# Performance work log

Hardware: AMD Instinct MI355X
Metric: run time of the kernel (lower is better)

## Reference

```python
import jax, jax.numpy as jnp
import numpy as np

FORGET_BIAS = 1.0  # TF BasicLSTMCell default


def setup_inputs() -> dict:
    key = jax.random.key(0)
    k1, k2, k3 = jax.random.split(key, 3)
    B, T, F, H = 4096, 512, 32, 60
    x = jax.random.normal(k1, (B, T, F), dtype=jnp.float32)
    # BasicLSTMCell kernel: [F+H, 4H], gate order i, j, f, o
    kernel = jax.random.normal(k2, (F + H, 4 * H), dtype=jnp.float32) * 0.1
    bias = jnp.zeros((4 * H,), dtype=jnp.float32)
    dense_w = jax.random.normal(k3, (H, 1), dtype=jnp.float32) * 0.1
    dense_b = jnp.zeros((1,), dtype=jnp.float32)
    return {"x": x, "kernel": kernel, "bias": bias,
            "dense_w": dense_w, "dense_b": dense_b}


def reference(x, kernel, bias, dense_w, dense_b):
    B, T, F = x.shape
    H = dense_w.shape[0]

    def step(carry, x_t):
        c, h = carry  # each [B, H]
        gates = jnp.concatenate([x_t, h], axis=1) @ kernel + bias  # [B, 4H]
        i, j, f, o = jnp.split(gates, 4, axis=1)
        new_c = c * jax.nn.sigmoid(f + FORGET_BIAS) + jax.nn.sigmoid(i) * jnp.tanh(j)
        new_h = jnp.tanh(new_c) * jax.nn.sigmoid(o)
        return (new_c, new_h), None

    c0 = jnp.zeros((B, H), dtype=x.dtype)
    h0 = jnp.zeros((B, H), dtype=x.dtype)
    xs = jnp.transpose(x, (1, 0, 2))  # [T, B, F]
    (c, h), _ = jax.lax.scan(step, (c0, h0), xs)
    return h @ dense_w + dense_b  # [B, 1]
```

## Files before the change

### kernel.cpp

```cpp
#include <hip/hip_runtime.h>

typedef short short8  __attribute__((ext_vector_type(8)));
typedef float f32x4   __attribute__((ext_vector_type(4)));

#define B_TOTAL 4096
#define T_STEPS 512
#define F_IN    32
#define H_DIM   60
#define KW      92
#define BC      16
#define HPITCH  72

#define MFMA(A, B, C) __builtin_amdgcn_mfma_f32_16x16x32_bf16((A), (B), (C), 0, 0, 0)

__device__ __forceinline__ unsigned short bf16rne(float f) {
    unsigned int u = __float_as_uint(f);
    u += 0x7FFFu + ((u >> 16) & 1u);
    return (unsigned short)(u >> 16);
}
__device__ __forceinline__ float bf16tof(unsigned short s) {
    return __uint_as_float(((unsigned int)s) << 16);
}
__device__ __forceinline__ float rcpf(float z) {
    return __builtin_amdgcn_rcpf(z);
}
__device__ __forceinline__ float exp2f_(float z) {
#if __has_builtin(__builtin_amdgcn_exp2f)
    return __builtin_amdgcn_exp2f(z);
#else
    float r; asm("v_exp_f32 %0, %1" : "=v"(r) : "v"(z)); return r;
#endif
}

#define BAR()                                                                   \
    {                                                                           \
        asm volatile("s_waitcnt lgkmcnt(0)" ::: "memory");                      \
        __builtin_amdgcn_sched_barrier(0);                                      \
        __builtin_amdgcn_s_barrier();                                           \
        __builtin_amdgcn_sched_barrier(0);                                      \
    }

#define CVTH(VA, VB, OH)                                                        \
    {                                                                           \
        int4 hp;                                                                \
        asm("v_cvt_pk_bf16_f32 %0, %1, %2" : "=v"(hp.x) : "v"((VA).x), "v"((VA).y)); \
        asm("v_cvt_pk_bf16_f32 %0, %1, %2" : "=v"(hp.y) : "v"((VA).z), "v"((VA).w)); \
        asm("v_cvt_pk_bf16_f32 %0, %1, %2" : "=v"(hp.z) : "v"((VB).x), "v"((VB).y)); \
        asm("v_cvt_pk_bf16_f32 %0, %1, %2" : "=v"(hp.w) : "v"((VB).z), "v"((VB).w)); \
        OH = __builtin_bit_cast(short8, hp);                                    \
    }

#define CELL2(P, Q, H0, H1)                                                     \
    float h0, h1;                                                               \
    {                                                                           \
        float ei0 = exp2f_(-P[0]), ei1 = exp2f_(-Q[0]);                         \
        float qj0 = exp2f_(P[1]),  qj1 = exp2f_(Q[1]);                          \
        float ef0 = exp2f_(-P[2]), ef1 = exp2f_(-Q[2]);                         \
        float D10 = (1.0f + ei0) * (qj0 + 1.0f);                                \
        float D11 = (1.0f + ei1) * (qj1 + 1.0f);                                \
        float r1  = rcpf(D10 * D11);                                            \
        float D20 = 1.0f + ef0, D21 = 1.0f + ef1;                               \
        float r2  = rcpf(D20 * D21);                                            \
        cst0 = cst0 * (D21 * r2) + (qj0 - 1.0f) * (D11 * r1);                   \
        cst1 = cst1 * (D20 * r2) + (qj1 - 1.0f) * (D10 * r1);                   \
        float zc0 = __builtin_amdgcn_fmed3f(cst0 * (2.0f * 1.44269504088896340736f), -126.0f, 126.0f); \
        float zc1 = __builtin_amdgcn_fmed3f(cst1 * (2.0f * 1.44269504088896340736f), -126.0f, 126.0f); \
        float qc0 = exp2f_(zc0), qc1 = exp2f_(zc1);                             \
        float eo0 = exp2f_(-P[3]), eo1 = exp2f_(-Q[3]);                         \
        H0 = (qc0 - 1.0f) * rcpf((qc0 + 1.0f) * (1.0f + eo0));                  \
        H1 = (qc1 - 1.0f) * rcpf((qc1 + 1.0f) * (1.0f + eo1));                  \
    }

__global__ __launch_bounds__(512, 2)
void lstm_mfma_kernel(const float* __restrict__ x,
                      const float* __restrict__ wk,
                      const float* __restrict__ bias,
                      const float* __restrict__ dense_w,
                      const float* __restrict__ dense_b,
                      float* __restrict__ out)
{
    __shared__ __align__(16) short Hhi[2][BC][HPITCH];
    __shared__ float Hf[BC][64];

    const int tid  = threadIdx.x;
    const int lane = tid & 63;
    const int w    = tid >> 6;
    const int b0   = blockIdx.x * BC;
    const int lm   = lane & 15;
    const int kg   = lane >> 4;
    const int lk8  = kg * 8;

    const float LOG2E = 1.44269504088896340736f;

    short8 wh[2][3], wl[2][3];
    f32x4  biasv[2];
    #pragma unroll
    for (int tt = 0; tt < 2; ++tt) {
        const int mt = 2 * w + tt;
        if (mt < 15) {
            const int uo = 4 * mt + kg;
            f32x4 bv;
            #pragma unroll
            for (int r = 0; r < 4; ++r) {
                const float sc = (r == 1) ? 2.0f * LOG2E : LOG2E;
                bv[r] = (bias[r * 60 + uo] + (r == 2 ? 1.0f : 0.0f)) * sc;
            }
            biasv[tt] = bv;
            const int c = 16 * mt + lm;
            const int u = c >> 2, g = c & 3;
            const float gsc = (g == 1) ? 2.0f * LOG2E : LOG2E;
            #pragma unroll
            for (int s = 0; s < 3; ++s) {
                short8 hv, lv;
                #pragma unroll
                for (int e = 0; e < 8; ++e) {
                    const int k = s * 32 + lk8 + e;
                    float wv = (k < KW) ? wk[k * 240 + g * 60 + u] * gsc : 0.0f;
                    unsigned short hh = bf16rne(wv);
                    hv[e] = (short)hh;
                    lv[e] = (short)bf16rne(wv - bf16tof(hh));
                }
                wh[tt][s] = hv;
                wl[tt][s] = lv;
            }
        } else {
            biasv[tt] = (f32x4){0.f, 0.f, 0.f, 0.f};
            #pragma unroll
            for (int s = 0; s < 3; ++s) { wh[tt][s] = (short8)0; wl[tt][s] = (short8)0; }
        }
    }
    const int u0 = 8 * w + kg;
    const int u1 = 8 * w + 4 + kg;
    const bool t1ok = (2 * w + 1 < 15);

    for (int i = tid; i < 2 * BC * HPITCH; i += 512)
        (&Hhi[0][0][0])[i] = 0;

    const float* xrow = x + (size_t)(b0 + lm) * (T_STEPS * F_IN) + lk8;
    float4 va0 = *reinterpret_cast<const float4*>(xrow);
    float4 vb0 = *reinterpret_cast<const float4*>(xrow + 4);
    short8 axh;
    CVTH(va0, vb0, axh)
    float4 sBa = *reinterpret_cast<const float4*>(xrow + 1 * F_IN);
    float4 sBb = *reinterpret_cast<const float4*>(xrow + 1 * F_IN + 4);
    float4 sAa, sAb;
    const float* xp2 = xrow + 2 * F_IN;

    float cst0 = 0.f, cst1 = 0.f;
    __syncthreads();

#define STEPX(CUR, NXT, DOLOAD, LA, LB, XOFF, DOCVT, CA, CB, LASTF)             \
    {                                                                           \
        short8 uh1 = *reinterpret_cast<const short8*>(&Hhi[CUR][lm][lk8]);      \
        short8 uh2 = *reinterpret_cast<const short8*>(&Hhi[CUR][lm][32 + lk8]); \
        if (DOLOAD) {                                                           \
            LA = *reinterpret_cast<const float4*>(xp2 + (XOFF));                \
            LB = *reinterpret_cast<const float4*>(xp2 + (XOFF) + 4);            \
        }                                                                       \
        __builtin_amdgcn_s_setprio(1);                                          \
        f32x4 p = MFMA(wh[0][0], axh, biasv[0]);                                \
        f32x4 q = MFMA(wh[1][0], axh, biasv[1]);                                \
        p = MFMA(wh[0][1], uh1, p);                                             \
        q = MFMA(wh[1][1], uh1, q);                                             \
        p = MFMA(wl[0][1], uh1, p);                                             \
        q = MFMA(wl[1][1], uh1, q);                                             \
        p = MFMA(wh[0][2], uh2, p);                                             \
        q = MFMA(wh[1][2], uh2, q);                                             \
        p = MFMA(wl[0][2], uh2, p);                                             \
        q = MFMA(wl[1][2], uh2, q);                                             \
        __builtin_amdgcn_s_setprio(0);                                          \
        CELL2(p, q, h0, h1)                                                     \
        int pk;                                                                 \
        asm("v_cvt_pk_bf16_f32 %0, %1, %2" : "=v"(pk) : "v"(h0), "v"(h1));      \
        if (LASTF) {                                                            \
            Hf[lm][u0] = h0;                                                    \
            if (t1ok) Hf[lm][u1] = h1;                                          \
        } else {                                                                \
            Hhi[NXT][lm][u0] = (short)pk;                                       \
            if (t1ok) Hhi[NXT][lm][u1] = (short)(((unsigned)pk) >> 16);         \
        }                                                                       \
        if (DOCVT) CVTH(CA, CB, axh)                                            \
        BAR()                                                                   \
    }

    for (int t = 0; t < T_STEPS - 2; t += 2) {
        STEPX(0, 1, 1, sAa, sAb, 0,    1, sBa, sBb, 0)
        STEPX(1, 0, 1, sBa, sBb, F_IN, 1, sAa, sAb, 0)
        xp2 += 2 * F_IN;
    }
    STEPX(0, 1, 0, sAa, sAb, 0, 1, sBa, sBb, 0)
    STEPX(1, 0, 0, sAa, sAb, 0, 0, sBa, sBb, 1)

    if (tid < BC) {
        float acc = dense_b[0];
        #pragma unroll 4
        for (int uu = 0; uu < H_DIM; ++uu)
            acc = fmaf(Hf[tid][uu], dense_w[uu], acc);
        out[b0 + tid] = acc;
    }
}

extern "C" void kernel_launch(void* const* d_in, const int* in_sizes, int n_in,
                              void* d_out, int out_size, void* d_ws, size_t ws_size,
                              hipStream_t stream) {
    const float* x       = (const float*)d_in[0];
    const float* wk      = (const float*)d_in[1];
    const float* bias    = (const float*)d_in[2];
    const float* dense_w = (const float*)d_in[3];
    const float* dense_b = (const float*)d_in[4];
    float* out = (float*)d_out;

    lstm_mfma_kernel<<<B_TOTAL / BC, 512, 0, stream>>>(
        x, wk, bias, dense_w, dense_b, out);
}
```

Baseline: 238.9 us.

## Drop bf16 low-part weight split and pack h pairs into single LDS store

Removes the hi/lo bf16 split of the recurrent weights, so each step runs 6 MFMAs instead of 10. The hidden-state buffer is reordered so each lane's two h values sit next to each other and go out as one 32-bit LDS store, and the weight columns are permuted to match. The s_setprio hints around the MFMA block are also removed. This shortens the serial per-timestep critical path, but the recurrent matmul weights lose precision, which can raise numerical error over 512 steps.

```diff
diff --git a/kernel.cpp b/kernel.cpp
--- a/kernel.cpp
+++ b/kernel.cpp
@@ -17,9 +17,6 @@
     unsigned int u = __float_as_uint(f);
     u += 0x7FFFu + ((u >> 16) & 1u);
     return (unsigned short)(u >> 16);
-}
-__device__ __forceinline__ float bf16tof(unsigned short s) {
-    return __uint_as_float(((unsigned int)s) << 16);
 }
 __device__ __forceinline__ float rcpf(float z) {
     return __builtin_amdgcn_rcpf(z);
@@ -92,7 +89,7 @@
 
     const float LOG2E = 1.44269504088896340736f;
 
-    short8 wh[2][3], wl[2][3];
+    short8 wh[2][3];
     f32x4  biasv[2];
     #pragma unroll
     for (int tt = 0; tt < 2; ++tt) {
@@ -109,28 +106,35 @@
             const int c = 16 * mt + lm;
             const int u = c >> 2, g = c & 3;
             const float gsc = (g == 1) ? 2.0f * LOG2E : LOG2E;
+            {
+                short8 hv;
+                #pragma unroll
+                for (int e = 0; e < 8; ++e)
+                    hv[e] = (short)bf16rne(wk[(lk8 + e) * 240 + g * 60 + u] * gsc);
+                wh[tt][0] = hv;
+            }
             #pragma unroll
-            for (int s = 0; s < 3; ++s) {
-                short8 hv, lv;
+            for (int s = 1; s < 3; ++s) {
+                short8 hv;
                 #pragma unroll
                 for (int e = 0; e < 8; ++e) {
-                    const int k = s * 32 + lk8 + e;
-                    float wv = (k < KW) ? wk[k * 240 + g * 60 + u] * gsc : 0.0f;
-                    unsigned short hh = bf16rne(wv);
-                    hv[e] = (short)hh;
-                    lv[e] = (short)bf16rne(wv - bf16tof(hh));
+                    const int cc = (s - 1) * 32 + lk8 + e;
+                    const int m  = cc >> 1, bit = cc & 1;
+                    const int uk = 8 * (m >> 2) + 4 * bit + (m & 3);
+                    float wv = (uk < H_DIM) ? wk[(F_IN + uk) * 240 + g * 60 + u] * gsc : 0.0f;
+                    hv[e] = (short)bf16rne(wv);
                 }
                 wh[tt][s] = hv;
-                wl[tt][s] = lv;
             }
         } else {
             biasv[tt] = (f32x4){0.f, 0.f, 0.f, 0.f};
             #pragma unroll
-            for (int s = 0; s < 3; ++s) { wh[tt][s] = (short8)0; wl[tt][s] = (short8)0; }
+            for (int s = 0; s < 3; ++s) wh[tt][s] = (short8)0;
         }
     }
     const int u0 = 8 * w + kg;
     const int u1 = 8 * w + 4 + kg;
+    const int mIdx = 4 * w + kg;
     const bool t1ok = (2 * w + 1 < 15);
 
     for (int i = tid; i < 2 * BC * HPITCH; i += 512)
@@ -157,18 +161,12 @@
             LA = *reinterpret_cast<const float4*>(xp2 + (XOFF));                \
             LB = *reinterpret_cast<const float4*>(xp2 + (XOFF) + 4);            \
         }                                                                       \
-        __builtin_amdgcn_s_setprio(1);                                          \
         f32x4 p = MFMA(wh[0][0], axh, biasv[0]);                                \
         f32x4 q = MFMA(wh[1][0], axh, biasv[1]);                                \
         p = MFMA(wh[0][1], uh1, p);                                             \
         q = MFMA(wh[1][1], uh1, q);                                             \
-        p = MFMA(wl[0][1], uh1, p);                                             \
-        q = MFMA(wl[1][1], uh1, q);                                             \
         p = MFMA(wh[0][2], uh2, p);                                             \
         q = MFMA(wh[1][2], uh2, q);                                             \
-        p = MFMA(wl[0][2], uh2, p);                                             \
-        q = MFMA(wl[1][2], uh2, q);                                             \
-        __builtin_amdgcn_s_setprio(0);                                          \
         CELL2(p, q, h0, h1)                                                     \
         int pk;                                                                 \
         asm("v_cvt_pk_bf16_f32 %0, %1, %2" : "=v"(pk) : "v"(h0), "v"(h1));      \
@@ -176,8 +174,7 @@
             Hf[lm][u0] = h0;                                                    \
             if (t1ok) Hf[lm][u1] = h1;                                          \
         } else {                                                                \
-            Hhi[NXT][lm][u0] = (short)pk;                                       \
-            if (t1ok) Hhi[NXT][lm][u1] = (short)(((unsigned)pk) >> 16);         \
+            *reinterpret_cast<int*>(&Hhi[NXT][lm][2 * mIdx]) = pk;              \
         }                                                                       \
         if (DOCVT) CVTH(CA, CB, axh)                                            \
         BAR()                                                                   \
```

New measurement: 284.8 us. 1.19x slower.
